# Kernel tuning notes

Measured on AMD Instinct MI355X. Metric: run time of the kernel, lower is better.

Reference implementation:

```python
import jax, jax.numpy as jnp
import numpy as np

D_MODEL = 1024
HEADS = 16
DK = D_MODEL // HEADS
B, S = 2, 2048


def setup_inputs() -> dict:
    key = jax.random.key(0)
    ks = jax.random.split(key, 9)
    s = 0.02
    return {
        "Q": jax.random.normal(ks[0], (B, S, D_MODEL), jnp.float32),
        "K": jax.random.normal(ks[1], (B, S, D_MODEL), jnp.float32),
        "V": jax.random.normal(ks[2], (B, S, D_MODEL), jnp.float32),
        "mask": jnp.ones((B, 1, S), jnp.int32),
        "Wq": jax.random.normal(ks[3], (D_MODEL, D_MODEL), jnp.float32) * s,
        "Wk": jax.random.normal(ks[4], (D_MODEL, D_MODEL), jnp.float32) * s,
        "Wv": jax.random.normal(ks[5], (D_MODEL, D_MODEL), jnp.float32) * s,
        "Wo": jax.random.normal(ks[6], (D_MODEL, D_MODEL), jnp.float32) * s,
        "ln_gamma": jnp.ones((D_MODEL,), jnp.float32),
        "ln_beta": jnp.zeros((D_MODEL,), jnp.float32),
    }


def _layer_norm(x, gamma, beta, eps=1e-5):
    mu = jnp.mean(x, axis=-1, keepdims=True)
    var = jnp.mean(jnp.square(x - mu), axis=-1, keepdims=True)
    return (x - mu) * jax.lax.rsqrt(var + eps) * gamma + beta


def reference(Q, K, V, mask, Wq, Wk, Wv, Wo, ln_gamma, ln_beta):
    # torch Linear(no bias): y = x @ W.T
    def split_heads(x):  # [B,S,D] -> [B,H,S,dk]
        return x.reshape(B, -1, HEADS, DK).transpose(0, 2, 1, 3)

    q = split_heads(Q @ Wq.T)
    k = split_heads(K @ Wk.T)
    v = split_heads(V @ Wv.T)

    # scores: [B,H,Sq,Sk]
    scores = jnp.einsum("bhqd,bhkd->bhqk", q, k) / np.sqrt(DK).astype(np.float32)
    m = mask[:, None, :, :]  # [B,1,1,S] broadcast over heads and queries
    scores = jnp.where(m == 0, -jnp.inf, scores)
    attn = jax.nn.softmax(scores, axis=-1)  # dropout is identity in eval
    out = jnp.einsum("bhqk,bhkd->bhqd", attn, v)
    out = out.transpose(0, 2, 1, 3).reshape(B, -1, D_MODEL)
    out = out @ Wo.T
    return _layer_norm(out + Q, ln_gamma, ln_beta)
```

## Files before the change

### kernel.cpp

```cpp
#include <hip/hip_runtime.h>
#include <hip/hip_bf16.h>
#include <stdint.h>

#define NB 2
#define NS 2048
#define ND 1024
#define NH 16
#define NDK 64
#define NM (NB*NS)

using bf16x8 = __attribute__((ext_vector_type(8))) short;
using f32x4  = __attribute__((ext_vector_type(4))) float;
using f32x16 = __attribute__((ext_vector_type(16))) float;
using u32x4  = __attribute__((ext_vector_type(4))) unsigned;

__device__ __forceinline__ unsigned short f2bf(float f){
  unsigned u = __float_as_uint(f);
  u += 0x7fffu + ((u>>16)&1u);
  return (unsigned short)(u>>16);
}

__device__ __forceinline__ void gload_lds16(const void* g, void* l){
  __builtin_amdgcn_global_load_lds((const __attribute__((address_space(1))) void*)g,
                                   (__attribute__((address_space(3))) void*)l, 16, 0, 0);
}

__device__ __forceinline__ float fexp2(float x){
#if __has_builtin(__builtin_amdgcn_exp2f)
  return __builtin_amdgcn_exp2f(x);
#else
  return __expf(x * 0.69314718056f);
#endif
}

__device__ __forceinline__ unsigned cvtpk_bf16(float lo, float hi){
  unsigned r;
  asm("v_cvt_pk_bf16_f32 %0, %1, %2" : "=v"(r) : "v"(lo), "v"(hi));
  return r;
}

__device__ __forceinline__ void swap32(unsigned &a, unsigned &b){
#if __has_builtin(__builtin_amdgcn_permlane32_swap)
  auto rr = __builtin_amdgcn_permlane32_swap((int)a, (int)b, false, false);
  a = (unsigned)rr[0]; b = (unsigned)rr[1];
#else
  const bool lo = (threadIdx.x & 32) == 0;
  unsigned sa = (unsigned)__shfl_xor((int)a, 32, 64);
  unsigned sb = (unsigned)__shfl_xor((int)b, 32, 64);
  unsigned na = lo ? a : sb;
  unsigned nb = lo ? sa : b;
  a = na; b = nb;
#endif
}

__device__ __forceinline__ f32x16 mfma32(bf16x8 a, bf16x8 b, f32x16 c){
  return __builtin_amdgcn_mfma_f32_32x32x16_bf16(a, b, c, 0, 0, 0);
}

__global__ __launch_bounds__(256) void prep_k(const float* __restrict__ Q, const float* __restrict__ K,
                                              const float* __restrict__ V, const float* __restrict__ Wq,
                                              const float* __restrict__ Wk, const float* __restrict__ Wv,
                                              const float* __restrict__ Wo,
                                              unsigned short* __restrict__ Xbf,
                                              unsigned short* __restrict__ Wbf){
  const int bid = blockIdx.x;
  const float* src; unsigned short* dst; int i;
  if (bid < 12288){
    const int which = bid >> 12;
    src = (which==0) ? Q : (which==1) ? K : V;
    dst = Xbf + ((size_t)which << 22);
    i = (bid & 4095)*256 + threadIdx.x;
  } else {
    const int which = (bid - 12288) >> 10;
    src = (which==0) ? Wq : (which==1) ? Wk : (which==2) ? Wv : Wo;
    dst = Wbf + ((size_t)which << 20);
    i = ((bid - 12288) & 1023)*256 + threadIdx.x;
  }
  float4 v = ((const float4*)src)[i];
  ushort4 o;
  o.x = f2bf(v.x); o.y = f2bf(v.y); o.z = f2bf(v.z); o.w = f2bf(v.w);
  ((ushort4*)dst)[i] = o;
}

__global__ __launch_bounds__(256) void gemm_qkv(const short* __restrict__ Xbf, const short* __restrict__ Wbf,
                                                unsigned short* __restrict__ qh, unsigned short* __restrict__ kh,
                                                unsigned short* __restrict__ vT){
  __shared__ short lsA[2][4096];
  __shared__ short lsB[2][4096];
  const int tid = threadIdx.x;
  const int hw = blockIdx.x;
  const int logical = (hw & 7)*96 + (hw >> 3);
  const int z = logical >> 8, rem = logical & 255;
  const int my = rem >> 3, nx = rem & 7;
  const short* A = Xbf + (size_t)z*NM*ND;
  const short* W = Wbf + (size_t)z*ND*ND;
  unsigned short* out = (z==0) ? qh : (z==1) ? kh : vT;
  const int mode = (z==2) ? 1 : 0;
  const int m0 = my*128, n0 = nx*128;

  const short* gA = A + (size_t)m0*1024;
  const short* gB = W + (size_t)n0*1024;
  const int srow = tid>>2, scol = (tid&3)*8;
  const int w = tid>>6, lane = tid&63, lr = lane&15, lk = lane>>4;
  const int wm = w>>1, wn = w&1;

  f32x4 acc[4][4];
  #pragma unroll
  for (int i=0;i<4;++i)
    #pragma unroll
    for (int j=0;j<4;++j) acc[i][j] = (f32x4){0.f,0.f,0.f,0.f};

  #pragma unroll
  for (int r=0;r<2;++r){
    gload_lds16(gA + (size_t)(r*64+srow)*1024 + scol, &lsA[0][(r*256+tid)*8]);
    gload_lds16(gB + (size_t)(r*64+srow)*1024 + scol, &lsB[0][(r*256+tid)*8]);
  }
  int cur = 0;
  for (int ks=0; ks<32; ++ks){
    __syncthreads();
    if (ks+1 < 32){
      const int k0 = (ks+1)*32;
      #pragma unroll
      for (int r=0;r<2;++r){
        gload_lds16(gA + (size_t)(r*64+srow)*1024 + k0 + scol, &lsA[cur^1][(r*256+tid)*8]);
        gload_lds16(gB + (size_t)(r*64+srow)*1024 + k0 + scol, &lsB[cur^1][(r*256+tid)*8]);
      }
    }
    bf16x8 af[4], bfr[4];
    #pragma unroll
    for (int i=0;i<4;++i){
      af[i]  = *(const bf16x8*)&lsA[cur][(wm*64+i*16+lr)*32 + lk*8];
      bfr[i] = *(const bf16x8*)&lsB[cur][(wn*64+i*16+lr)*32 + lk*8];
    }
    #pragma unroll
    for (int i=0;i<4;++i)
      #pragma unroll
      for (int j=0;j<4;++j)
        acc[i][j] = __builtin_amdgcn_mfma_f32_16x16x32_bf16(af[i], bfr[j], acc[i][j], 0,0,0);
    cur ^= 1;
  }
  #pragma unroll
  for (int i=0;i<4;++i)
    #pragma unroll
    for (int j=0;j<4;++j)
      #pragma unroll
      for (int r=0;r<4;++r){
        const int m = m0 + wm*64 + i*16 + lk*4 + r;
        const int n = n0 + wn*64 + j*16 + lr;
        const float v = acc[i][j][r];
        const int b = m>>11, s = m&2047, h = n>>6, dk = n&63;
        size_t addr;
        if (mode == 0) addr = (((size_t)(b*NH+h))*NS + s)*NDK + dk;
        else           addr = (((size_t)(b*NH+h))*NDK + dk)*NS + s;
        out[addr] = f2bf(v);
      }
}

__global__ __launch_bounds__(256) void gemm_out(const short* __restrict__ Attn, const short* __restrict__ Wo,
                                                const float* __restrict__ Qin, float* __restrict__ proj){
  __shared__ short lsA[2][4096];
  __shared__ short lsB[2][4096];
  const int tid = threadIdx.x;
  const int hw = blockIdx.x;
  const int logical = (hw & 7)*32 + (hw >> 3);
  const int my = logical >> 3, nx = logical & 7;
  const int m0 = my*128, n0 = nx*128;
  const short* gA = Attn + (size_t)m0*1024;
  const short* gB = Wo + (size_t)n0*1024;
  const int srow = tid>>2, scol = (tid&3)*8;
  const int w = tid>>6, lane = tid&63, lr = lane&15, lk = lane>>4;
  const int wm = w>>1, wn = w&1;

  f32x4 acc[4][4];
  #pragma unroll
  for (int i=0;i<4;++i)
    #pragma unroll
    for (int j=0;j<4;++j) acc[i][j] = (f32x4){0.f,0.f,0.f,0.f};

  #pragma unroll
  for (int r=0;r<2;++r){
    gload_lds16(gA + (size_t)(r*64+srow)*1024 + scol, &lsA[0][(r*256+tid)*8]);
    gload_lds16(gB + (size_t)(r*64+srow)*1024 + scol, &lsB[0][(r*256+tid)*8]);
  }
  int cur = 0;
  for (int ks=0; ks<32; ++ks){
    __syncthreads();
    if (ks+1 < 32){
      const int k0 = (ks+1)*32;
      #pragma unroll
      for (int r=0;r<2;++r){
        gload_lds16(gA + (size_t)(r*64+srow)*1024 + k0 + scol, &lsA[cur^1][(r*256+tid)*8]);
        gload_lds16(gB + (size_t)(r*64+srow)*1024 + k0 + scol, &lsB[cur^1][(r*256+tid)*8]);
      }
    }
    bf16x8 af[4], bfr[4];
    #pragma unroll
    for (int i=0;i<4;++i){
      af[i]  = *(const bf16x8*)&lsA[cur][(wm*64+i*16+lr)*32 + lk*8];
      bfr[i] = *(const bf16x8*)&lsB[cur][(wn*64+i*16+lr)*32 + lk*8];
    }
    #pragma unroll
    for (int i=0;i<4;++i)
      #pragma unroll
      for (int j=0;j<4;++j)
        acc[i][j] = __builtin_amdgcn_mfma_f32_16x16x32_bf16(af[i], bfr[j], acc[i][j], 0,0,0);
    cur ^= 1;
  }
  #pragma unroll
  for (int i=0;i<4;++i)
    #pragma unroll
    for (int j=0;j<4;++j)
      #pragma unroll
      for (int r=0;r<4;++r){
        const int m = m0 + wm*64 + i*16 + lk*4 + r;
        const int n = n0 + wn*64 + j*16 + lr;
        proj[(size_t)m*1024 + n] = acc[i][j][r] + Qin[(size_t)m*1024 + n];
      }
}

__global__ __launch_bounds__(512) void attn_k(const short* __restrict__ qh, const short* __restrict__ kh,
                                              const short* __restrict__ vT, const int* __restrict__ mask,
                                              unsigned short* __restrict__ attn){
  __shared__ char sb[66048];
  const int bid = blockIdx.x;
  const int qb = bid & 15, h = (bid>>4)&15, b = bid>>8;
  const int tid = threadIdx.x, w = tid>>6, lane = tid&63;
  const int ql = lane & 31, hi = lane>>5;
  const int qw = w & 3, half = w>>2;
  const int bh = b*NH + h;
  const int q0 = qb*128 + qw*32;
  const float C2 = 0.18033688f;

  const int D = tid*16;
  const int strow = D>>7;
  const int S = D ^ ((strow&7)<<4);
  const char* ksrc = (const char*)(kh + (size_t)bh*NS*NDK) + S;
  const char* vsrc = (const char*)(vT + ((size_t)bh*NDK + strow)*NS) + (S & 127);

  const short* qrow = qh + ((size_t)bh*NS + q0 + ql)*NDK + hi*8;
  bf16x8 qf[4];
  #pragma unroll
  for (int kp=0;kp<4;++kp) qf[kp] = *(const bf16x8*)(qrow + kp*16);

  const int* mrow = mask + b*NS;
  unsigned long long* smask = (unsigned long long*)(sb + 65536);

  gload_lds16(ksrc,                      sb + D);
  gload_lds16(ksrc + (size_t)1024*128,   sb + 8192 + D);
  gload_lds16(vsrc,                      sb + 32768 + D);
  gload_lds16(vsrc + (size_t)1024*2,     sb + 32768 + 8192 + D);

  #pragma unroll
  for (int j=0;j<4;++j){
    const int gt = w*4 + j;
    const unsigned long long bal = __ballot(mrow[gt*64 + lane] != 0);
    if (lane == 0) smask[gt] = bal;
  }

  f32x16 o0, o1;
  #pragma unroll
  for (int r=0;r<16;++r){ o0[r]=0.f; o1[r]=0.f; }
  float mrun = -1e30f, lrun = 0.f;

  const int swz = (ql&7)<<4;

  for (int t=0; t<16; ++t){
    const int buf = (t&1)*16384;
    __syncthreads();
    if (t+1 < 16){
      const int nbuf = ((t+1)&1)*16384;
      const size_t kvn0 = (size_t)(t+1)*64, kvn1 = 1024 + kvn0;
      gload_lds16(ksrc + kvn0*128, sb + nbuf + D);
      gload_lds16(ksrc + kvn1*128, sb + nbuf + 8192 + D);
      gload_lds16(vsrc + kvn0*2,   sb + 32768 + nbuf + D);
      gload_lds16(vsrc + kvn1*2,   sb + 32768 + nbuf + 8192 + D);
    }
    const unsigned long long m64 = smask[half*16 + t];
    const unsigned mw0 = (unsigned)m64, mw1 = (unsigned)(m64>>32);
    const bool allm = (~m64) == 0ull;

    const char* kb = sb + buf + half*8192;
    const char* vb = sb + 32768 + buf + half*8192;

    bf16x8 kf[8];
    #pragma unroll
    for (int kvh=0;kvh<2;++kvh)
      #pragma unroll
      for (int kp=0;kp<4;++kp)
        kf[kvh*4+kp] = *(const bf16x8*)(kb + (((kvh*32+ql)*128 + kp*32 + hi*16) ^ swz));

    f32x16 s0, s1;
    #pragma unroll
    for (int r=0;r<16;++r){ s0[r]=0.f; s1[r]=0.f; }
    #pragma unroll
    for (int kp=0;kp<4;++kp){
      s0 = mfma32(kf[kp],   qf[kp], s0);
      s1 = mfma32(kf[4+kp], qf[kp], s1);
    }

    float t16[16];
    #pragma unroll
    for (int r=0;r<16;++r) t16[r] = fmaxf(s0[r], s1[r]);
    #pragma unroll
    for (int st=8; st>=1; st>>=1)
      #pragma unroll
      for (int r=0;r<st;++r) t16[r] = fmaxf(t16[r], t16[r+st]);
    const float tm = fmaxf(t16[0], __shfl_xor(t16[0], 32, 64));

    if (!__all(tm - mrun <= 32.f)){
      const float mnew = fmaxf(mrun, tm);
      const float fac  = fexp2((mrun - mnew)*C2);
      mrun = mnew;
      #pragma unroll
      for (int r=0;r<16;++r){ o0[r]*=fac; o1[r]*=fac; }
      lrun *= fac;
    }
    const float nb = mrun*C2;

    bf16x8 vf[8];
    #pragma unroll
    for (int dh=0;dh<2;++dh)
      #pragma unroll
      for (int c=0;c<4;++c)
        vf[dh*4+c] = *(const bf16x8*)(vb + (((dh*32+ql)*128 + c*32 + hi*16) ^ swz));

    float psum = 0.f;
    #pragma unroll
    for (int kvh=0; kvh<2; ++kvh){
      const f32x16& ss = kvh ? s1 : s0;
      const unsigned mw = kvh ? mw1 : mw0;
      unsigned pwd[8];
      float ps0 = 0.f, ps1 = 0.f;
      #pragma unroll
      for (int i=0;i<8;++i){
        const int bp0 = ((2*i)&3) + 8*((2*i)>>2);
        float p0 = fexp2(ss[2*i]*C2   - nb);
        float p1 = fexp2(ss[2*i+1]*C2 - nb);
        if (!allm){
          p0 = ((mw >> (bp0     + 4*hi)) & 1u) ? p0 : 0.f;
          p1 = ((mw >> (bp0 + 1 + 4*hi)) & 1u) ? p1 : 0.f;
        }
        ps0 += p0; ps1 += p1;
        pwd[i] = cvtpk_bf16(p0, p1);
      }
      psum += ps0 + ps1;
      swap32(pwd[0], pwd[2]);
      swap32(pwd[1], pwd[3]);
      swap32(pwd[4], pwd[6]);
      swap32(pwd[5], pwd[7]);
      u32x4 c0w = {pwd[0], pwd[1], pwd[2], pwd[3]};
      u32x4 c1w = {pwd[4], pwd[5], pwd[6], pwd[7]};
      bf16x8 pf0 = __builtin_bit_cast(bf16x8, c0w);
      bf16x8 pf1 = __builtin_bit_cast(bf16x8, c1w);
      o0 = mfma32(vf[2*kvh],       pf0, o0);
      o1 = mfma32(vf[4 + 2*kvh],   pf0, o1);
      o0 = mfma32(vf[2*kvh + 1],   pf1, o0);
      o1 = mfma32(vf[4 + 2*kvh+1], pf1, o1);
    }
    psum += __shfl_xor(psum, 32, 64);
    lrun += psum;
  }

  __syncthreads();
  float* smm = (float*)(sb + 32768);
  float* sml = (float*)(sb + 32768 + 1024);
  if (hi == 0){ smm[w*32 + ql] = mrun; sml[w*32 + ql] = lrun; }
  __syncthreads();
  const float pmv = smm[(w^4)*32 + ql], plv = sml[(w^4)*32 + ql];
  const float mfin = fmaxf(mrun, pmv);
  const float facS = fexp2((mrun - mfin)*C2);
  if (w >= 4){
    float* eg = (float*)(sb + (size_t)(w-4)*8192);
    #pragma unroll
    for (int r=0;r<16;++r){
      eg[ql + 32*(hi*16 + r)]        = o0[r]*facS;
      eg[ql + 32*(hi*16 + r) + 1024] = o1[r]*facS;
    }
  }
  __syncthreads();
  if (w < 4){
    float* eg = (float*)(sb + (size_t)w*8192);
    #pragma unroll
    for (int r=0;r<16;++r){
      o0[r] = o0[r]*facS + eg[ql + 32*(hi*16 + r)];
      o1[r] = o1[r]*facS + eg[ql + 32*(hi*16 + r) + 1024];
    }
    const float facP = fexp2((pmv - mfin)*C2);
    const float lfin = lrun*facS + plv*facP;
    const float inv = 1.f / lfin;
    asm volatile("s_waitcnt lgkmcnt(0)" ::: "memory");
    char* ep = sb + (size_t)w*8192;
    #pragma unroll
    for (int dh=0; dh<2; ++dh){
      const f32x16& oo = dh ? o1 : o0;
      #pragma unroll
      for (int i=0;i<8;++i){
        const int d0 = ((2*i)&3) + 8*((2*i)>>2) + 4*hi + dh*32;
        const unsigned pk = cvtpk_bf16(oo[2*i]*inv, oo[2*i+1]*inv);
        *(unsigned*)(ep + (((ql*128) + d0*2) ^ ((ql&7)<<4))) = pk;
      }
    }
    asm volatile("s_waitcnt lgkmcnt(0)" ::: "memory");
    #pragma unroll
    for (int seg=0; seg<4; ++seg){
      const int qq = seg*8 + (lane>>3), dc = (lane&7)*8;
      bf16x8 vv = *(const bf16x8*)(ep + (((qq*128) + dc*2) ^ ((qq&7)<<4)));
      *(bf16x8*)(attn + ((size_t)b*NS + q0 + qq)*ND + h*NDK + dc) = vv;
    }
  }
}

__global__ __launch_bounds__(256) void ln_k(const float* __restrict__ proj,
                                            const float* __restrict__ gamma, const float* __restrict__ beta,
                                            float* __restrict__ out){
  const int row = blockIdx.x*4 + (threadIdx.x>>6);
  const int lane = threadIdx.x & 63;
  const float4* pp = (const float4*)(proj + (size_t)row*ND);
  float4 x[4];
  float sum = 0.f;
  #pragma unroll
  for (int i=0;i<4;++i){
    x[i] = pp[lane + i*64];
    sum += x[i].x + x[i].y + x[i].z + x[i].w;
  }
  #pragma unroll
  for (int off=32; off>=1; off>>=1) sum += __shfl_xor(sum, off, 64);
  const float mu = sum * (1.f/1024.f);
  float vs = 0.f;
  #pragma unroll
  for (int i=0;i<4;++i){
    float d0=x[i].x-mu, d1=x[i].y-mu, d2=x[i].z-mu, d3=x[i].w-mu;
    vs += d0*d0 + d1*d1 + d2*d2 + d3*d3;
  }
  #pragma unroll
  for (int off=32; off>=1; off>>=1) vs += __shfl_xor(vs, off, 64);
  const float rstd = rsqrtf(vs*(1.f/1024.f) + 1e-5f);
  #pragma unroll
  for (int i=0;i<4;++i){
    const float4 g  = ((const float4*)gamma)[lane + i*64];
    const float4 be = ((const float4*)beta)[lane + i*64];
    float4 y;
    y.x = (x[i].x-mu)*rstd*g.x + be.x;
    y.y = (x[i].y-mu)*rstd*g.y + be.y;
    y.z = (x[i].z-mu)*rstd*g.z + be.z;
    y.w = (x[i].w-mu)*rstd*g.w + be.w;
    ((float4*)(out + (size_t)row*ND))[lane + i*64] = y;
  }
}

extern "C" void kernel_launch(void* const* d_in, const int* in_sizes, int n_in,
                              void* d_out, int out_size, void* d_ws, size_t ws_size,
                              hipStream_t stream){
  const float* Q    = (const float*)d_in[0];
  const float* K    = (const float*)d_in[1];
  const float* V    = (const float*)d_in[2];
  const int*   mask = (const int*)  d_in[3];
  const float* Wq   = (const float*)d_in[4];
  const float* Wk   = (const float*)d_in[5];
  const float* Wv   = (const float*)d_in[6];
  const float* Wo   = (const float*)d_in[7];
  const float* gam  = (const float*)d_in[8];
  const float* bet  = (const float*)d_in[9];
  float* out = (float*)d_out;
  char* ws = (char*)d_ws;

  unsigned short* Wbf  = (unsigned short*)(ws);
  unsigned short* Xbf  = (unsigned short*)(ws + (size_t)(8u<<20));
  unsigned short* qhp  = (unsigned short*)(ws + (size_t)(32u<<20));
  unsigned short* khp  = (unsigned short*)(ws + (size_t)(40u<<20));
  unsigned short* vTp  = (unsigned short*)(ws + (size_t)(48u<<20));
  unsigned short* attb = (unsigned short*)(ws + (size_t)(56u<<20));
  float* proj  = (float*)(ws + (size_t)(8u<<20));

  prep_k<<<16384,256,0,stream>>>(Q, K, V, Wq, Wk, Wv, Wo, Xbf, Wbf);

  gemm_qkv<<<768,256,0,stream>>>((const short*)Xbf, (const short*)Wbf, qhp, khp, vTp);

  attn_k<<<512,512,0,stream>>>((const short*)qhp, (const short*)khp, (const short*)vTp, mask, attb);

  gemm_out<<<256,256,0,stream>>>((const short*)attb, (const short*)(Wbf + (3u<<20)), Q, proj);

  ln_k<<<1024,256,0,stream>>>(proj, gam, bet, out);
}
```

Before: 173.2 us.

## Fuse fp32-to-bf16 activation conversion into QKV GEMM and tweak attention scheduling

```diff
diff --git a/kernel.cpp b/kernel.cpp
--- a/kernel.cpp
+++ b/kernel.cpp
@@ -57,50 +57,41 @@
   return __builtin_amdgcn_mfma_f32_32x32x16_bf16(a, b, c, 0, 0, 0);
 }
 
-__global__ __launch_bounds__(256) void prep_k(const float* __restrict__ Q, const float* __restrict__ K,
-                                              const float* __restrict__ V, const float* __restrict__ Wq,
-                                              const float* __restrict__ Wk, const float* __restrict__ Wv,
-                                              const float* __restrict__ Wo,
-                                              unsigned short* __restrict__ Xbf,
+__global__ __launch_bounds__(256) void prep_k(const float* __restrict__ Wq, const float* __restrict__ Wk,
+                                              const float* __restrict__ Wv, const float* __restrict__ Wo,
                                               unsigned short* __restrict__ Wbf){
   const int bid = blockIdx.x;
-  const float* src; unsigned short* dst; int i;
-  if (bid < 12288){
-    const int which = bid >> 12;
-    src = (which==0) ? Q : (which==1) ? K : V;
-    dst = Xbf + ((size_t)which << 22);
-    i = (bid & 4095)*256 + threadIdx.x;
-  } else {
-    const int which = (bid - 12288) >> 10;
-    src = (which==0) ? Wq : (which==1) ? Wk : (which==2) ? Wv : Wo;
-    dst = Wbf + ((size_t)which << 20);
-    i = ((bid - 12288) & 1023)*256 + threadIdx.x;
-  }
+  const int which = bid >> 10;
+  const float* src = (which==0) ? Wq : (which==1) ? Wk : (which==2) ? Wv : Wo;
+  unsigned short* dst = Wbf + ((size_t)which << 20);
+  const int i = (bid & 1023)*256 + threadIdx.x;
   float4 v = ((const float4*)src)[i];
   ushort4 o;
   o.x = f2bf(v.x); o.y = f2bf(v.y); o.z = f2bf(v.z); o.w = f2bf(v.w);
   ((ushort4*)dst)[i] = o;
 }
 
-__global__ __launch_bounds__(256) void gemm_qkv(const short* __restrict__ Xbf, const short* __restrict__ Wbf,
+__global__ __launch_bounds__(256) void gemm_qkv(const float* __restrict__ Qf, const float* __restrict__ Kf,
+                                                const float* __restrict__ Vf, const short* __restrict__ Wbf,
                                                 unsigned short* __restrict__ qh, unsigned short* __restrict__ kh,
                                                 unsigned short* __restrict__ vT){
-  __shared__ short lsA[2][4096];
+  __shared__ float lsA[2][4096];
   __shared__ short lsB[2][4096];
   const int tid = threadIdx.x;
   const int hw = blockIdx.x;
   const int logical = (hw & 7)*96 + (hw >> 3);
   const int z = logical >> 8, rem = logical & 255;
   const int my = rem >> 3, nx = rem & 7;
-  const short* A = Xbf + (size_t)z*NM*ND;
+  const float* A = (z==0) ? Qf : (z==1) ? Kf : Vf;
   const short* W = Wbf + (size_t)z*ND*ND;
   unsigned short* out = (z==0) ? qh : (z==1) ? kh : vT;
   const int mode = (z==2) ? 1 : 0;
   const int m0 = my*128, n0 = nx*128;
 
-  const short* gA = A + (size_t)m0*1024;
+  const float* gA = A + (size_t)m0*1024;
   const short* gB = W + (size_t)n0*1024;
-  const int srow = tid>>2, scol = (tid&3)*8;
+  const int bsrow = tid>>2, bscol = (tid&3)*8;
+  const int asrow = tid>>3, ascol = (tid&7)*4;
   const int w = tid>>6, lane = tid&63, lr = lane&15, lk = lane>>4;
   const int wm = w>>1, wn = w&1;
 
@@ -111,25 +102,33 @@
     for (int j=0;j<4;++j) acc[i][j] = (f32x4){0.f,0.f,0.f,0.f};
 
   #pragma unroll
-  for (int r=0;r<2;++r){
-    gload_lds16(gA + (size_t)(r*64+srow)*1024 + scol, &lsA[0][(r*256+tid)*8]);
-    gload_lds16(gB + (size_t)(r*64+srow)*1024 + scol, &lsB[0][(r*256+tid)*8]);
-  }
+  for (int r=0;r<4;++r)
+    gload_lds16(gA + (size_t)(r*32+asrow)*1024 + ascol, &lsA[0][r*1024 + asrow*32 + ascol]);
+  #pragma unroll
+  for (int r=0;r<2;++r)
+    gload_lds16(gB + (size_t)(r*64+bsrow)*1024 + bscol, &lsB[0][(r*256+tid)*8]);
+
   int cur = 0;
   for (int ks=0; ks<32; ++ks){
     __syncthreads();
     if (ks+1 < 32){
       const int k0 = (ks+1)*32;
       #pragma unroll
-      for (int r=0;r<2;++r){
-        gload_lds16(gA + (size_t)(r*64+srow)*1024 + k0 + scol, &lsA[cur^1][(r*256+tid)*8]);
-        gload_lds16(gB + (size_t)(r*64+srow)*1024 + k0 + scol, &lsB[cur^1][(r*256+tid)*8]);
-      }
+      for (int r=0;r<4;++r)
+        gload_lds16(gA + (size_t)(r*32+asrow)*1024 + k0 + ascol, &lsA[cur^1][r*1024 + asrow*32 + ascol]);
+      #pragma unroll
+      for (int r=0;r<2;++r)
+        gload_lds16(gB + (size_t)(r*64+bsrow)*1024 + k0 + bscol, &lsB[cur^1][(r*256+tid)*8]);
     }
     bf16x8 af[4], bfr[4];
     #pragma unroll
     for (int i=0;i<4;++i){
-      af[i]  = *(const bf16x8*)&lsA[cur][(wm*64+i*16+lr)*32 + lk*8];
+      const float* ap = &lsA[cur][(wm*64+i*16+lr)*32 + lk*8];
+      const float4 lo = *(const float4*)ap;
+      const float4 hi = *(const float4*)(ap+4);
+      u32x4 aw = { cvtpk_bf16(lo.x, lo.y), cvtpk_bf16(lo.z, lo.w),
+                   cvtpk_bf16(hi.x, hi.y), cvtpk_bf16(hi.z, hi.w) };
+      af[i] = __builtin_bit_cast(bf16x8, aw);
       bfr[i] = *(const bf16x8*)&lsB[cur][(wn*64+i*16+lr)*32 + lk*8];
     }
     #pragma unroll
@@ -221,9 +220,10 @@
 __global__ __launch_bounds__(512) void attn_k(const short* __restrict__ qh, const short* __restrict__ kh,
                                               const short* __restrict__ vT, const int* __restrict__ mask,
                                               unsigned short* __restrict__ attn){
-  __shared__ char sb[66048];
-  const int bid = blockIdx.x;
-  const int qb = bid & 15, h = (bid>>4)&15, b = bid>>8;
+  __shared__ char sb[65536];
+  const int hw = blockIdx.x;
+  const int logical = (hw & 7)*64 + (hw >> 3);
+  const int qb = logical & 15, h = (logical>>4)&15, b = logical>>8;
   const int tid = threadIdx.x, w = tid>>6, lane = tid&63;
   const int ql = lane & 31, hi = lane>>5;
   const int qw = w & 3, half = w>>2;
@@ -242,20 +242,12 @@
   #pragma unroll
   for (int kp=0;kp<4;++kp) qf[kp] = *(const bf16x8*)(qrow + kp*16);
 
-  const int* mrow = mask + b*NS;
-  unsigned long long* smask = (unsigned long long*)(sb + 65536);
+  const int* mrow = mask + b*NS + half*1024;
 
   gload_lds16(ksrc,                      sb + D);
   gload_lds16(ksrc + (size_t)1024*128,   sb + 8192 + D);
   gload_lds16(vsrc,                      sb + 32768 + D);
   gload_lds16(vsrc + (size_t)1024*2,     sb + 32768 + 8192 + D);
-
-  #pragma unroll
-  for (int j=0;j<4;++j){
-    const int gt = w*4 + j;
-    const unsigned long long bal = __ballot(mrow[gt*64 + lane] != 0);
-    if (lane == 0) smask[gt] = bal;
-  }
 
   f32x16 o0, o1;
   #pragma unroll
@@ -275,9 +267,9 @@
       gload_lds16(vsrc + kvn0*2,   sb + 32768 + nbuf + D);
       gload_lds16(vsrc + kvn1*2,   sb + 32768 + nbuf + 8192 + D);
     }
-    const unsigned long long m64 = smask[half*16 + t];
-    const unsigned mw0 = (unsigned)m64, mw1 = (unsigned)(m64>>32);
-    const bool allm = (~m64) == 0ull;
+    const unsigned long long bal = __ballot(mrow[t*64 + lane] != 0);
+    const unsigned mw0 = (unsigned)bal, mw1 = (unsigned)(bal>>32);
+    const bool allm = (~bal) == 0ull;
 
     const char* kb = sb + buf + half*8192;
     const char* vb = sb + 32768 + buf + half*8192;
@@ -292,11 +284,13 @@
     f32x16 s0, s1;
     #pragma unroll
     for (int r=0;r<16;++r){ s0[r]=0.f; s1[r]=0.f; }
+    __builtin_amdgcn_s_setprio(1);
     #pragma unroll
     for (int kp=0;kp<4;++kp){
       s0 = mfma32(kf[kp],   qf[kp], s0);
       s1 = mfma32(kf[4+kp], qf[kp], s1);
     }
+    __builtin_amdgcn_s_setprio(0);
 
     float t16[16];
     #pragma unroll
@@ -352,10 +346,12 @@
       u32x4 c1w = {pwd[4], pwd[5], pwd[6], pwd[7]};
       bf16x8 pf0 = __builtin_bit_cast(bf16x8, c0w);
       bf16x8 pf1 = __builtin_bit_cast(bf16x8, c1w);
+      __builtin_amdgcn_s_setprio(1);
       o0 = mfma32(vf[2*kvh],       pf0, o0);
       o1 = mfma32(vf[4 + 2*kvh],   pf0, o1);
       o0 = mfma32(vf[2*kvh + 1],   pf1, o0);
       o1 = mfma32(vf[4 + 2*kvh+1], pf1, o1);
+      __builtin_amdgcn_s_setprio(0);
     }
     psum += __shfl_xor(psum, 32, 64);
     lrun += psum;
@@ -465,16 +461,15 @@
   char* ws = (char*)d_ws;
 
   unsigned short* Wbf  = (unsigned short*)(ws);
-  unsigned short* Xbf  = (unsigned short*)(ws + (size_t)(8u<<20));
   unsigned short* qhp  = (unsigned short*)(ws + (size_t)(32u<<20));
   unsigned short* khp  = (unsigned short*)(ws + (size_t)(40u<<20));
   unsigned short* vTp  = (unsigned short*)(ws + (size_t)(48u<<20));
   unsigned short* attb = (unsigned short*)(ws + (size_t)(56u<<20));
   float* proj  = (float*)(ws + (size_t)(8u<<20));
 
-  prep_k<<<16384,256,0,stream>>>(Q, K, V, Wq, Wk, Wv, Wo, Xbf, Wbf);
-
-  gemm_qkv<<<768,256,0,stream>>>((const short*)Xbf, (const short*)Wbf, qhp, khp, vTp);
+  prep_k<<<4096,256,0,stream>>>(Wq, Wk, Wv, Wo, Wbf);
+
+  gemm_qkv<<<768,256,0,stream>>>(Q, K, V, (const short*)Wbf, qhp, khp, vTp);
 
   attn_k<<<512,512,0,stream>>>((const short*)qhp, (const short*)khp, (const short*)vTp, mask, attb);
 
```

After: 166.4 us. -4.0%, faster.
